# Kernel optimization log

Measured on AMD Instinct MI355X. Metric: run time of the kernel, lower is better.

## Reference

```python
import jax, jax.numpy as jnp
import numpy as np

HIDDEN = 512
LAYERS = 3
K = 8
EPS = 1e-5


def build_adjacency(coords, k):
    # squared pairwise distances (monotone in cdist, so same top-k indices)
    sq = jnp.sum(coords * coords, axis=-1)                      # [B,N]
    d2 = sq[:, :, None] + sq[:, None, :] - 2.0 * jnp.einsum('bnc,bmc->bnm', coords, coords)
    _, idx = jax.lax.top_k(-d2, k + 1)                          # smallest k+1
    idx = idx[:, :, 1:]                                         # drop self  [B,N,k]
    B, N = coords.shape[:2]
    bidx = jnp.arange(B)[:, None, None]
    ridx = jnp.arange(N)[None, :, None]
    adj = jnp.zeros((B, N, N), coords.dtype).at[bidx, ridx, idx].set(1.0)
    adj = adj + jnp.swapaxes(adj, -2, -1)                       # symmetrize
    return (adj > 0).astype(coords.dtype)


def layer_norm(x, g, b):
    mu = jnp.mean(x, axis=-1, keepdims=True)
    var = jnp.var(x, axis=-1, keepdims=True)  # biased, matches torch LayerNorm
    return (x - mu) * jax.lax.rsqrt(var + EPS) * g + b


def setup_inputs() -> dict:
    key = jax.random.key(0)
    k1, k2, k3, k4 = jax.random.split(key, 4)
    B, N, H, L = 4, 4096, HIDDEN, LAYERS
    node_features = jax.random.normal(k1, (B, N, H), dtype=jnp.float32)
    coordinates = jax.random.uniform(k2, (B, N, 2), dtype=jnp.float32)
    scale = 1.0 / np.sqrt(H)
    W = jax.random.uniform(k3, (L, H, H), dtype=jnp.float32, minval=-scale, maxval=scale)
    b = jax.random.uniform(k4, (L, H), dtype=jnp.float32, minval=-scale, maxval=scale)
    gamma = jnp.ones((L, H), dtype=jnp.float32)
    beta = jnp.zeros((L, H), dtype=jnp.float32)
    return {"node_features": node_features, "coordinates": coordinates,
            "W": W, "b": b, "gamma": gamma, "beta": beta}


def reference(node_features, coordinates, W, b, gamma, beta):
    adj = build_adjacency(coordinates, K)                       # [B,N,N]
    x = node_features
    for i in range(LAYERS):
        x_new = jnp.einsum('bnm,bmh->bnh', adj, x)              # dense aggregate
        x_new = x_new @ W[i] + b[i]                             # linear
        x_new = jax.nn.relu(layer_norm(x_new, gamma[i], beta[i]))
        x = x + x_new if i > 0 else x_new
    return x
```

## Files before the change

kernel.cpp:

```cpp
#include <hip/hip_runtime.h>
#include <stdint.h>

#define HIDDEN 512
#define NLAYERS 3
#define KNN 8
#define CAP 64
#define EPSV 1e-5f
#define GRID 32
#define NCELL (GRID * GRID)

typedef unsigned long long u64;
typedef __attribute__((ext_vector_type(8))) short short8;
typedef __attribute__((ext_vector_type(4))) float f32x4;

__device__ inline unsigned short f2bf(float x) {
  union { float f; unsigned u; } v; v.f = x;
  unsigned r = v.u + 0x7FFFu + ((v.u >> 16) & 1u);
  return (unsigned short)(r >> 16);
}
__device__ inline float bf2f(unsigned short u) {
  return __uint_as_float((unsigned)u << 16);
}

__global__ __launch_bounds__(1024) void grid_build_kernel(
    const float2* __restrict__ coords, int* __restrict__ cell_start,
    float2* __restrict__ scoord, int* __restrict__ sorig, int N) {
  __shared__ int hist[NCELL];
  __shared__ int offs[NCELL];
  int b = blockIdx.x;
  int t = threadIdx.x;
  hist[t] = 0;
  __syncthreads();
  const float2* cb = coords + (size_t)b * N;
  int mycell[4];
#pragma unroll
  for (int r = 0; r < 4; ++r) {
    int i = t + r * 1024;
    float2 c = cb[i];
    int cx = (int)(c.x * GRID); cx = cx < 0 ? 0 : (cx > GRID - 1 ? GRID - 1 : cx);
    int cy = (int)(c.y * GRID); cy = cy < 0 ? 0 : (cy > GRID - 1 ? GRID - 1 : cy);
    mycell[r] = cy * GRID + cx;
    atomicAdd(&hist[mycell[r]], 1);
  }
  __syncthreads();
  int v = hist[t];
  offs[t] = v;
  __syncthreads();
  for (int d = 1; d < NCELL; d <<= 1) {
    int add = (t >= d) ? offs[t - d] : 0;
    __syncthreads();
    offs[t] += add;
    __syncthreads();
  }
  int excl = offs[t] - v;
  cell_start[(size_t)b * (NCELL + 1) + t] = excl;
  if (t == 0) cell_start[(size_t)b * (NCELL + 1) + NCELL] = N;
  hist[t] = excl;
  __syncthreads();
#pragma unroll
  for (int r = 0; r < 4; ++r) {
    int i = t + r * 1024;
    int pos = atomicAdd(&hist[mycell[r]], 1);
    scoord[(size_t)b * N + pos] = cb[i];
    sorig[(size_t)b * N + pos] = i;
  }
}

__global__ __launch_bounds__(256) void knn_grid_kernel(
    const int* __restrict__ cell_start, const float2* __restrict__ scoord,
    const int* __restrict__ sorig, int* __restrict__ knn_s, int N, int BN) {
  int gang = (blockIdx.x * blockDim.x + threadIdx.x) >> 3;
  int sub = threadIdx.x & 7;
  if (gang >= BN) return;
  int b = gang / N;
  float2 cn = scoord[gang];
  float sqn = __fmaf_rn(cn.y, cn.y, __fmul_rn(cn.x, cn.x));
  int cx = (int)(cn.x * GRID); cx = cx < 0 ? 0 : (cx > GRID - 1 ? GRID - 1 : cx);
  int cy = (int)(cn.y * GRID); cy = cy < 0 ? 0 : (cy > GRID - 1 ? GRID - 1 : cy);
  const int* cs = cell_start + (size_t)b * (NCELL + 1);
  const float2* sc = scoord + (size_t)b * N;
  const int* so = sorig + (size_t)b * N;

  u64 list[KNN + 1];
#pragma unroll
  for (int j = 0; j <= KNN; ++j) list[j] = ~0ull;

  auto scan_cell = [&](int ux, int uy) {
    int c = uy * GRID + ux;
    int s = cs[c], e = cs[c + 1];
    for (int p = s + sub; p < e; p += 8) {
      float2 cm = sc[p];
      float sqm = __fmaf_rn(cm.y, cm.y, __fmul_rn(cm.x, cm.x));
      float dot = __fmaf_rn(cn.y, cm.y, __fmul_rn(cn.x, cm.x));
      float d2 = __fsub_rn(__fadd_rn(sqn, sqm), __fmul_rn(2.0f, dot));
      unsigned ub = __float_as_uint(d2);
      unsigned k32 = (ub & 0x80000000u) ? ~ub : (ub | 0x80000000u);
      u64 key = ((u64)k32 << 24) | ((u64)(unsigned)so[p] << 12) | (u64)(unsigned)p;
      if (key < list[KNN]) {
        u64 cur = key;
#pragma unroll
        for (int j = 0; j <= KNN; ++j) {
          u64 lo = list[j] < cur ? list[j] : cur;
          u64 hi = list[j] < cur ? cur : list[j];
          list[j] = lo;
          cur = hi;
        }
      }
    }
  };

  for (int q = 0; q <= GRID; ++q) {
    if (q == 0) {
      scan_cell(cx, cy);
    } else {
      int x0 = cx - q, x1 = cx + q, y0 = cy - q, y1 = cy + q;
      int xa = x0 < 0 ? 0 : x0, xb_ = x1 > GRID - 1 ? GRID - 1 : x1;
      for (int ux = xa; ux <= xb_; ++ux) {
        if (y0 >= 0) scan_cell(ux, y0);
        if (y1 <= GRID - 1) scan_cell(ux, y1);
      }
      int ya = (y0 + 1) < 0 ? 0 : y0 + 1, yb = (y1 - 1) > GRID - 1 ? GRID - 1 : y1 - 1;
      for (int uy = ya; uy <= yb; ++uy) {
        if (x0 >= 0) scan_cell(x0, uy);
        if (x1 <= GRID - 1) scan_cell(x1, uy);
      }
      float bound = (float)q * (1.0f / GRID);
      float thr = bound * bound - 1e-5f;
      int cntn = 0;
#pragma unroll
      for (int j = 0; j <= KNN; ++j) {
        unsigned k32 = (unsigned)(list[j] >> 24);
        float d2v = (k32 >= 0x80000000u) ? __uint_as_float(k32 & 0x7FFFFFFFu)
                                         : -__uint_as_float(~k32);
        cntn += (list[j] != ~0ull && d2v < thr) ? 1 : 0;
      }
#pragma unroll
      for (int o = 1; o < 8; o <<= 1) cntn += __shfl_xor(cntn, o, 64);
      if (cntn >= 9) break;
    }
  }

  for (int r = 0; r <= KNN; ++r) {
    u64 cand = list[0];
    u64 mn = cand;
#pragma unroll
    for (int o = 1; o < 8; o <<= 1) {
      u64 v = __shfl_xor(mn, o, 64);
      mn = v < mn ? v : mn;
    }
    if (cand == mn) {
#pragma unroll
      for (int j = 0; j < KNN; ++j) list[j] = list[j + 1];
      list[KNN] = ~0ull;
      if (r > 0) knn_s[(size_t)gang * KNN + (r - 1)] = (int)(mn & 0xFFFull);
    }
  }
}

__global__ __launch_bounds__(256) void rev_build_kernel(const int* __restrict__ knn,
                                                        int* __restrict__ cnt,
                                                        int* __restrict__ rev,
                                                        int N, int BN) {
  int e = blockIdx.x * blockDim.x + threadIdx.x;
  if (e >= BN * KNN) return;
  int bn = e >> 3;
  int m = knn[e];
  int b = bn / N;
  int gm = b * N + m;
  int pos = atomicAdd(&cnt[gm], 1);
  if (pos < CAP) rev[(size_t)gm * CAP + pos] = bn - b * N;
}

__global__ __launch_bounds__(128) void x2bf_perm_kernel(const float* __restrict__ x,
                                                        const int* __restrict__ sorig,
                                                        unsigned short* __restrict__ xs,
                                                        int N) {
  int row = blockIdx.x;
  int b = row / N;
  int src = b * N + sorig[row];
  int t = threadIdx.x;
  float4 v = ((const float4*)(x + (size_t)src * HIDDEN))[t];
  ushort4 o;
  o.x = f2bf(v.x); o.y = f2bf(v.y); o.z = f2bf(v.z); o.w = f2bf(v.w);
  ((ushort4*)(xs + (size_t)row * HIDDEN))[t] = o;
}

__global__ __launch_bounds__(128) void agg_kernel(const unsigned short* __restrict__ x,
                                                  const int* __restrict__ knn,
                                                  const int* __restrict__ cnt,
                                                  const int* __restrict__ rev,
                                                  unsigned short* __restrict__ aggb,
                                                  int N) {
  int bn = blockIdx.x;
  int b = bn / N;
  int t = threadIdx.x;
  const int* my = knn + (size_t)bn * KNN;
  int nb[KNN];
#pragma unroll
  for (int j = 0; j < KNN; ++j) nb[j] = my[j];
  const unsigned short* xb = x + (size_t)b * N * HIDDEN;
  float4 acc = {0.f, 0.f, 0.f, 0.f};
#pragma unroll
  for (int j = 0; j < KNN; ++j) {
    ushort4 v = ((const ushort4*)(xb + (size_t)nb[j] * HIDDEN))[t];
    acc.x += bf2f(v.x); acc.y += bf2f(v.y); acc.z += bf2f(v.z); acc.w += bf2f(v.w);
  }
  int indeg = cnt[bn];
  if (indeg > CAP) indeg = CAP;
  const int* rv = rev + (size_t)bn * CAP;
  for (int i = 0; i < indeg; ++i) {
    int r = rv[i];
    bool dup = false;
#pragma unroll
    for (int j = 0; j < KNN; ++j) dup = dup || (r == nb[j]);
    if (!dup) {
      ushort4 v = ((const ushort4*)(xb + (size_t)r * HIDDEN))[t];
      acc.x += bf2f(v.x); acc.y += bf2f(v.y); acc.z += bf2f(v.z); acc.w += bf2f(v.w);
    }
  }
  ushort4 o;
  o.x = f2bf(acc.x); o.y = f2bf(acc.y); o.z = f2bf(acc.z); o.w = f2bf(acc.w);
  ((ushort4*)(aggb + (size_t)bn * HIDDEN))[t] = o;
}

__global__ __launch_bounds__(256) void wconv_kernel(const float* __restrict__ W,
                                                    unsigned short* __restrict__ Wt) {
  __shared__ unsigned short tile[64][65];
  int l = blockIdx.x >> 6;
  int t6 = blockIdx.x & 63;
  int k0 = (t6 >> 3) * 64, n0 = (t6 & 7) * 64;
  const float* Wl = W + (size_t)l * HIDDEN * HIDDEN;
  unsigned short* Wtl = Wt + (size_t)l * HIDDEN * HIDDEN;
  int t = threadIdx.x;
#pragma unroll
  for (int r = 0; r < 4; ++r) {
    int row = (t >> 4) + r * 16;
    int col = (t & 15) * 4;
    float4 v = *(const float4*)(Wl + (size_t)(k0 + row) * HIDDEN + n0 + col);
    tile[col + 0][row] = f2bf(v.x);
    tile[col + 1][row] = f2bf(v.y);
    tile[col + 2][row] = f2bf(v.z);
    tile[col + 3][row] = f2bf(v.w);
  }
  __syncthreads();
#pragma unroll
  for (int r = 0; r < 4; ++r) {
    int row = (t >> 4) + r * 16;
    int col = (t & 15) * 4;
    ushort4 o;
    o.x = tile[row][col + 0]; o.y = tile[row][col + 1];
    o.z = tile[row][col + 2]; o.w = tile[row][col + 3];
    *(ushort4*)(Wtl + (size_t)(n0 + row) * HIDDEN + k0 + col) = o;
  }
}

__global__ __launch_bounds__(256) void gemm_mfma_kernel(
    const unsigned short* __restrict__ A,
    const unsigned short* __restrict__ Wt,
    const float* __restrict__ bias,
    float* __restrict__ C) {
  __shared__ unsigned short As[128 * 40];
  __shared__ unsigned short Bs[128 * 40];
  int t = threadIdx.x;
  int n0 = blockIdx.x * 128;
  int m0 = blockIdx.y * 128;
  int w = t >> 6, lane = t & 63;
  int wr = w >> 1, wc = w & 1;
  int lm = lane & 15, q = lane >> 4;

  f32x4 acc[4][4];
#pragma unroll
  for (int i = 0; i < 4; ++i)
#pragma unroll
    for (int j = 0; j < 4; ++j) acc[i][j] = (f32x4){0.f, 0.f, 0.f, 0.f};

  int srow = t >> 2;
  int scol = (t & 3) * 8;

  for (int k0 = 0; k0 < HIDDEN; k0 += 32) {
    uint4 a0 = *(const uint4*)(A + (size_t)(m0 + srow) * HIDDEN + k0 + scol);
    uint4 a1 = *(const uint4*)(A + (size_t)(m0 + srow + 64) * HIDDEN + k0 + scol);
    uint4 b0 = *(const uint4*)(Wt + (size_t)(n0 + srow) * HIDDEN + k0 + scol);
    uint4 b1 = *(const uint4*)(Wt + (size_t)(n0 + srow + 64) * HIDDEN + k0 + scol);
    __syncthreads();
    *(uint4*)(As + srow * 40 + scol) = a0;
    *(uint4*)(As + (srow + 64) * 40 + scol) = a1;
    *(uint4*)(Bs + srow * 40 + scol) = b0;
    *(uint4*)(Bs + (srow + 64) * 40 + scol) = b1;
    __syncthreads();
    short8 af[4], bfr[4];
#pragma unroll
    for (int i = 0; i < 4; ++i)
      af[i] = *(const short8*)(As + (wr * 64 + i * 16 + lm) * 40 + q * 8);
#pragma unroll
    for (int j = 0; j < 4; ++j)
      bfr[j] = *(const short8*)(Bs + (wc * 64 + j * 16 + lm) * 40 + q * 8);
#pragma unroll
    for (int i = 0; i < 4; ++i)
#pragma unroll
      for (int j = 0; j < 4; ++j)
        acc[i][j] = __builtin_amdgcn_mfma_f32_16x16x32_bf16(af[i], bfr[j], acc[i][j], 0, 0, 0);
  }

#pragma unroll
  for (int i = 0; i < 4; ++i) {
    int row = m0 + wr * 64 + i * 16 + q * 4;
#pragma unroll
    for (int j = 0; j < 4; ++j) {
      int col = n0 + wc * 64 + j * 16 + lm;
      float bv = bias[col];
#pragma unroll
      for (int r = 0; r < 4; ++r)
        C[(size_t)(row + r) * HIDDEN + col] = acc[i][j][r] + bv;
    }
  }
}

__global__ __launch_bounds__(256) void ln_relu_res_kernel(
    const float* __restrict__ t, const float* __restrict__ g,
    const float* __restrict__ be, unsigned short* __restrict__ xs,
    float* __restrict__ out, const int* __restrict__ sorig,
    int N, int addres, int final_) {
  int row = (blockIdx.x << 2) + (threadIdx.x >> 6);
  int lane = threadIdx.x & 63;
  const float4* tr = (const float4*)(t + (size_t)row * HIDDEN);
  float4 v0 = tr[lane];
  float4 v1 = tr[lane + 64];
  float s = ((v0.x + v0.y) + (v0.z + v0.w)) + ((v1.x + v1.y) + (v1.z + v1.w));
  float ss = ((v0.x * v0.x + v0.y * v0.y) + (v0.z * v0.z + v0.w * v0.w)) +
             ((v1.x * v1.x + v1.y * v1.y) + (v1.z * v1.z + v1.w * v1.w));
#pragma unroll
  for (int o = 32; o > 0; o >>= 1) {
    s += __shfl_xor(s, o, 64);
    ss += __shfl_xor(ss, o, 64);
  }
  float mu = s * (1.0f / HIDDEN);
  float var = ss * (1.0f / HIDDEN) - mu * mu;
  float inv = rsqrtf(var + EPSV);
  float4 g0 = ((const float4*)g)[lane], g1 = ((const float4*)g)[lane + 64];
  float4 b0 = ((const float4*)be)[lane], b1 = ((const float4*)be)[lane + 64];
  float4 o0, o1;
  o0.x = fmaxf((v0.x - mu) * inv * g0.x + b0.x, 0.f);
  o0.y = fmaxf((v0.y - mu) * inv * g0.y + b0.y, 0.f);
  o0.z = fmaxf((v0.z - mu) * inv * g0.z + b0.z, 0.f);
  o0.w = fmaxf((v0.w - mu) * inv * g0.w + b0.w, 0.f);
  o1.x = fmaxf((v1.x - mu) * inv * g1.x + b1.x, 0.f);
  o1.y = fmaxf((v1.y - mu) * inv * g1.y + b1.y, 0.f);
  o1.z = fmaxf((v1.z - mu) * inv * g1.z + b1.z, 0.f);
  o1.w = fmaxf((v1.w - mu) * inv * g1.w + b1.w, 0.f);
  ushort4* xrow = (ushort4*)(xs + (size_t)row * HIDDEN);
  if (addres) {
    ushort4 r0 = xrow[lane], r1 = xrow[lane + 64];
    o0.x += bf2f(r0.x); o0.y += bf2f(r0.y); o0.z += bf2f(r0.z); o0.w += bf2f(r0.w);
    o1.x += bf2f(r1.x); o1.y += bf2f(r1.y); o1.z += bf2f(r1.z); o1.w += bf2f(r1.w);
  }
  if (final_) {
    int b = row / N;
    int dst = b * N + sorig[row];
    float4* orow = (float4*)(out + (size_t)dst * HIDDEN);
    orow[lane] = o0;
    orow[lane + 64] = o1;
  } else {
    ushort4 q0, q1;
    q0.x = f2bf(o0.x); q0.y = f2bf(o0.y); q0.z = f2bf(o0.z); q0.w = f2bf(o0.w);
    q1.x = f2bf(o1.x); q1.y = f2bf(o1.y); q1.z = f2bf(o1.z); q1.w = f2bf(o1.w);
    xrow[lane] = q0;
    xrow[lane + 64] = q1;
  }
}

extern "C" void kernel_launch(void* const* d_in, const int* in_sizes, int n_in,
                              void* d_out, int out_size, void* d_ws, size_t ws_size,
                              hipStream_t stream) {
  const float* nf = (const float*)d_in[0];
  const float2* coords = (const float2*)d_in[1];
  const float* Wall = (const float*)d_in[2];
  const float* ball = (const float*)d_in[3];
  const float* gall = (const float*)d_in[4];
  const float* beall = (const float*)d_in[5];
  float* out = (float*)d_out;

  int BN = in_sizes[0] / HIDDEN;
  int N = 4096;
  int B = BN / N;

  char* ws = (char*)d_ws;
  size_t off = 0;
  auto alloc = [&](size_t bytes) -> void* {
    off = (off + 255) & ~(size_t)255;
    void* p = ws + off;
    off += bytes;
    return p;
  };
  int* knn_s = (int*)alloc((size_t)BN * KNN * sizeof(int));
  int* cnt = (int*)alloc((size_t)BN * sizeof(int));
  int* rev = (int*)alloc((size_t)BN * CAP * sizeof(int));
  unsigned short* aggb = (unsigned short*)alloc((size_t)BN * HIDDEN * sizeof(unsigned short));
  float* tmp = (float*)alloc((size_t)BN * HIDDEN * sizeof(float));
  unsigned short* Wt = (unsigned short*)alloc((size_t)NLAYERS * HIDDEN * HIDDEN * sizeof(unsigned short));
  unsigned short* xs = (unsigned short*)alloc((size_t)BN * HIDDEN * sizeof(unsigned short));
  int* cell_start = (int*)alloc((size_t)B * (NCELL + 1) * sizeof(int));
  float2* scoord = (float2*)alloc((size_t)BN * sizeof(float2));
  int* sorig = (int*)alloc((size_t)BN * sizeof(int));

  hipMemsetAsync(cnt, 0, (size_t)BN * sizeof(int), stream);
  grid_build_kernel<<<B, 1024, 0, stream>>>(coords, cell_start, scoord, sorig, N);
  knn_grid_kernel<<<(BN * 8 + 255) / 256, 256, 0, stream>>>(cell_start, scoord, sorig, knn_s, N, BN);
  rev_build_kernel<<<(BN * KNN) / 256, 256, 0, stream>>>(knn_s, cnt, rev, N, BN);
  wconv_kernel<<<NLAYERS * 64, 256, 0, stream>>>(Wall, Wt);
  x2bf_perm_kernel<<<BN, 128, 0, stream>>>(nf, sorig, xs, N);

  for (int l = 0; l < NLAYERS; ++l) {
    agg_kernel<<<BN, 128, 0, stream>>>(xs, knn_s, cnt, rev, aggb, N);
    gemm_mfma_kernel<<<dim3(HIDDEN / 128, BN / 128), 256, 0, stream>>>(
        aggb, Wt + (size_t)l * HIDDEN * HIDDEN, ball + (size_t)l * HIDDEN, tmp);
    ln_relu_res_kernel<<<BN / 4, 256, 0, stream>>>(
        tmp, gall + (size_t)l * HIDDEN, beall + (size_t)l * HIDDEN,
        xs, out, sorig, N, l > 0, l == NLAYERS - 1);
  }
}
```

Measured before the change: 296.4 us.

## Fuse GEMM with LayerNorm, ReLU and residual using full-row tiles

Replaces the separate GEMM and LayerNorm/ReLU/residual kernels with one kernel where each 512-thread block computes 64 full output rows across all 512 columns. Row statistics are reduced with shuffles and shared memory, then normalization, ReLU, residual add and output stores happen from registers. This removes the fp32 intermediate buffer's write and read plus a launch. In exchange, each block reloads the entire weight slice, the grid shrinks to fewer, larger blocks, and epilogue stores are narrow and strided.

```diff
diff --git a/kernel.cpp b/kernel.cpp
--- a/kernel.cpp
+++ b/kernel.cpp
@@ -254,18 +254,22 @@
   }
 }
 
-__global__ __launch_bounds__(256) void gemm_mfma_kernel(
+__global__ __launch_bounds__(512) void gemm_ln_fused_kernel(
     const unsigned short* __restrict__ A,
     const unsigned short* __restrict__ Wt,
     const float* __restrict__ bias,
-    float* __restrict__ C) {
-  __shared__ unsigned short As[128 * 40];
-  __shared__ unsigned short Bs[128 * 40];
+    const float* __restrict__ g,
+    const float* __restrict__ be,
+    unsigned short* __restrict__ xs,
+    float* __restrict__ out,
+    const int* __restrict__ sorig,
+    int N, int addres, int final_) {
+  __shared__ unsigned short As[64 * 40];
+  __shared__ unsigned short Bs[512 * 40];
+  __shared__ float red[8][64][2];
   int t = threadIdx.x;
-  int n0 = blockIdx.x * 128;
-  int m0 = blockIdx.y * 128;
+  int m0 = blockIdx.x * 64;
   int w = t >> 6, lane = t & 63;
-  int wr = w >> 1, wc = w & 1;
   int lm = lane & 15, q = lane >> 4;
 
   f32x4 acc[4][4];
@@ -274,98 +278,114 @@
 #pragma unroll
     for (int j = 0; j < 4; ++j) acc[i][j] = (f32x4){0.f, 0.f, 0.f, 0.f};
 
-  int srow = t >> 2;
-  int scol = (t & 3) * 8;
+  int arow = t >> 2;
+  int acol = (t & 3) * 8;
+  int brow0 = t >> 2;
+  int bcol = (t & 3) * 8;
 
   for (int k0 = 0; k0 < HIDDEN; k0 += 32) {
-    uint4 a0 = *(const uint4*)(A + (size_t)(m0 + srow) * HIDDEN + k0 + scol);
-    uint4 a1 = *(const uint4*)(A + (size_t)(m0 + srow + 64) * HIDDEN + k0 + scol);
-    uint4 b0 = *(const uint4*)(Wt + (size_t)(n0 + srow) * HIDDEN + k0 + scol);
-    uint4 b1 = *(const uint4*)(Wt + (size_t)(n0 + srow + 64) * HIDDEN + k0 + scol);
+    uint4 av;
+    if (t < 256) av = *(const uint4*)(A + (size_t)(m0 + arow) * HIDDEN + k0 + acol);
+    uint4 bv[4];
+#pragma unroll
+    for (int r = 0; r < 4; ++r)
+      bv[r] = *(const uint4*)(Wt + (size_t)(brow0 + r * 128) * HIDDEN + k0 + bcol);
     __syncthreads();
-    *(uint4*)(As + srow * 40 + scol) = a0;
-    *(uint4*)(As + (srow + 64) * 40 + scol) = a1;
-    *(uint4*)(Bs + srow * 40 + scol) = b0;
-    *(uint4*)(Bs + (srow + 64) * 40 + scol) = b1;
+    if (t < 256) *(uint4*)(As + arow * 40 + acol) = av;
+#pragma unroll
+    for (int r = 0; r < 4; ++r)
+      *(uint4*)(Bs + (brow0 + r * 128) * 40 + bcol) = bv[r];
     __syncthreads();
-    short8 af[4], bfr[4];
+    short8 af[4], bf[4];
 #pragma unroll
     for (int i = 0; i < 4; ++i)
-      af[i] = *(const short8*)(As + (wr * 64 + i * 16 + lm) * 40 + q * 8);
+      af[i] = *(const short8*)(As + (i * 16 + lm) * 40 + q * 8);
 #pragma unroll
     for (int j = 0; j < 4; ++j)
-      bfr[j] = *(const short8*)(Bs + (wc * 64 + j * 16 + lm) * 40 + q * 8);
+      bf[j] = *(const short8*)(Bs + (w * 64 + j * 16 + lm) * 40 + q * 8);
 #pragma unroll
     for (int i = 0; i < 4; ++i)
 #pragma unroll
       for (int j = 0; j < 4; ++j)
-        acc[i][j] = __builtin_amdgcn_mfma_f32_16x16x32_bf16(af[i], bfr[j], acc[i][j], 0, 0, 0);
-  }
+        acc[i][j] = __builtin_amdgcn_mfma_f32_16x16x32_bf16(af[i], bf[j], acc[i][j], 0, 0, 0);
+  }
+
+  float bv4[4], gv[4], bev[4];
+#pragma unroll
+  for (int j = 0; j < 4; ++j) {
+    int col = w * 64 + j * 16 + lm;
+    bv4[j] = bias[col]; gv[j] = g[col]; bev[j] = be[col];
+  }
+  float s[4][4], ss[4][4];
+#pragma unroll
+  for (int i = 0; i < 4; ++i)
+#pragma unroll
+    for (int r = 0; r < 4; ++r) { s[i][r] = 0.f; ss[i][r] = 0.f; }
+#pragma unroll
+  for (int i = 0; i < 4; ++i)
+#pragma unroll
+    for (int j = 0; j < 4; ++j)
+#pragma unroll
+      for (int r = 0; r < 4; ++r) {
+        float v = acc[i][j][r] + bv4[j];
+        acc[i][j][r] = v;
+        s[i][r] += v;
+        ss[i][r] += v * v;
+      }
+#pragma unroll
+  for (int i = 0; i < 4; ++i)
+#pragma unroll
+    for (int r = 0; r < 4; ++r) {
+#pragma unroll
+      for (int o = 1; o < 16; o <<= 1) {
+        s[i][r] += __shfl_xor(s[i][r], o, 64);
+        ss[i][r] += __shfl_xor(ss[i][r], o, 64);
+      }
+    }
+  if (lm == 0) {
+#pragma unroll
+    for (int i = 0; i < 4; ++i)
+#pragma unroll
+      for (int r = 0; r < 4; ++r) {
+        int rloc = i * 16 + q * 4 + r;
+        red[w][rloc][0] = s[i][r];
+        red[w][rloc][1] = ss[i][r];
+      }
+  }
+  __syncthreads();
 
 #pragma unroll
   for (int i = 0; i < 4; ++i) {
-    int row = m0 + wr * 64 + i * 16 + q * 4;
-#pragma unroll
-    for (int j = 0; j < 4; ++j) {
-      int col = n0 + wc * 64 + j * 16 + lm;
-      float bv = bias[col];
-#pragma unroll
-      for (int r = 0; r < 4; ++r)
-        C[(size_t)(row + r) * HIDDEN + col] = acc[i][j][r] + bv;
-    }
-  }
-}
-
-__global__ __launch_bounds__(256) void ln_relu_res_kernel(
-    const float* __restrict__ t, const float* __restrict__ g,
-    const float* __restrict__ be, unsigned short* __restrict__ xs,
-    float* __restrict__ out, const int* __restrict__ sorig,
-    int N, int addres, int final_) {
-  int row = (blockIdx.x << 2) + (threadIdx.x >> 6);
-  int lane = threadIdx.x & 63;
-  const float4* tr = (const float4*)(t + (size_t)row * HIDDEN);
-  float4 v0 = tr[lane];
-  float4 v1 = tr[lane + 64];
-  float s = ((v0.x + v0.y) + (v0.z + v0.w)) + ((v1.x + v1.y) + (v1.z + v1.w));
-  float ss = ((v0.x * v0.x + v0.y * v0.y) + (v0.z * v0.z + v0.w * v0.w)) +
-             ((v1.x * v1.x + v1.y * v1.y) + (v1.z * v1.z + v1.w * v1.w));
-#pragma unroll
-  for (int o = 32; o > 0; o >>= 1) {
-    s += __shfl_xor(s, o, 64);
-    ss += __shfl_xor(ss, o, 64);
-  }
-  float mu = s * (1.0f / HIDDEN);
-  float var = ss * (1.0f / HIDDEN) - mu * mu;
-  float inv = rsqrtf(var + EPSV);
-  float4 g0 = ((const float4*)g)[lane], g1 = ((const float4*)g)[lane + 64];
-  float4 b0 = ((const float4*)be)[lane], b1 = ((const float4*)be)[lane + 64];
-  float4 o0, o1;
-  o0.x = fmaxf((v0.x - mu) * inv * g0.x + b0.x, 0.f);
-  o0.y = fmaxf((v0.y - mu) * inv * g0.y + b0.y, 0.f);
-  o0.z = fmaxf((v0.z - mu) * inv * g0.z + b0.z, 0.f);
-  o0.w = fmaxf((v0.w - mu) * inv * g0.w + b0.w, 0.f);
-  o1.x = fmaxf((v1.x - mu) * inv * g1.x + b1.x, 0.f);
-  o1.y = fmaxf((v1.y - mu) * inv * g1.y + b1.y, 0.f);
-  o1.z = fmaxf((v1.z - mu) * inv * g1.z + b1.z, 0.f);
-  o1.w = fmaxf((v1.w - mu) * inv * g1.w + b1.w, 0.f);
-  ushort4* xrow = (ushort4*)(xs + (size_t)row * HIDDEN);
-  if (addres) {
-    ushort4 r0 = xrow[lane], r1 = xrow[lane + 64];
-    o0.x += bf2f(r0.x); o0.y += bf2f(r0.y); o0.z += bf2f(r0.z); o0.w += bf2f(r0.w);
-    o1.x += bf2f(r1.x); o1.y += bf2f(r1.y); o1.z += bf2f(r1.z); o1.w += bf2f(r1.w);
-  }
-  if (final_) {
-    int b = row / N;
-    int dst = b * N + sorig[row];
-    float4* orow = (float4*)(out + (size_t)dst * HIDDEN);
-    orow[lane] = o0;
-    orow[lane + 64] = o1;
-  } else {
-    ushort4 q0, q1;
-    q0.x = f2bf(o0.x); q0.y = f2bf(o0.y); q0.z = f2bf(o0.z); q0.w = f2bf(o0.w);
-    q1.x = f2bf(o1.x); q1.y = f2bf(o1.y); q1.z = f2bf(o1.z); q1.w = f2bf(o1.w);
-    xrow[lane] = q0;
-    xrow[lane + 64] = q1;
+#pragma unroll
+    for (int r = 0; r < 4; ++r) {
+      int rloc = i * 16 + q * 4 + r;
+      float S = 0.f, SS = 0.f;
+#pragma unroll
+      for (int ww = 0; ww < 8; ++ww) { S += red[ww][rloc][0]; SS += red[ww][rloc][1]; }
+      float mu = S * (1.0f / HIDDEN);
+      float var = SS * (1.0f / HIDDEN) - mu * mu;
+      float inv = rsqrtf(var + EPSV);
+      int row_g = m0 + rloc;
+      if (final_) {
+        int bb = row_g / N;
+        size_t dst = (size_t)(bb * N + sorig[row_g]) * HIDDEN;
+#pragma unroll
+        for (int j = 0; j < 4; ++j) {
+          int col = w * 64 + j * 16 + lm;
+          float v = fmaxf((acc[i][j][r] - mu) * inv * gv[j] + bev[j], 0.f);
+          if (addres) v += bf2f(xs[(size_t)row_g * HIDDEN + col]);
+          out[dst + col] = v;
+        }
+      } else {
+#pragma unroll
+        for (int j = 0; j < 4; ++j) {
+          int col = w * 64 + j * 16 + lm;
+          float v = fmaxf((acc[i][j][r] - mu) * inv * gv[j] + bev[j], 0.f);
+          if (addres) v += bf2f(xs[(size_t)row_g * HIDDEN + col]);
+          xs[(size_t)row_g * HIDDEN + col] = f2bf(v);
+        }
+      }
+    }
   }
 }
 
@@ -396,7 +416,6 @@
   int* cnt = (int*)alloc((size_t)BN * sizeof(int));
   int* rev = (int*)alloc((size_t)BN * CAP * sizeof(int));
   unsigned short* aggb = (unsigned short*)alloc((size_t)BN * HIDDEN * sizeof(unsigned short));
-  float* tmp = (float*)alloc((size_t)BN * HIDDEN * sizeof(float));
   unsigned short* Wt = (unsigned short*)alloc((size_t)NLAYERS * HIDDEN * HIDDEN * sizeof(unsigned short));
   unsigned short* xs = (unsigned short*)alloc((size_t)BN * HIDDEN * sizeof(unsigned short));
   int* cell_start = (int*)alloc((size_t)B * (NCELL + 1) * sizeof(int));
@@ -412,10 +431,9 @@
 
   for (int l = 0; l < NLAYERS; ++l) {
     agg_kernel<<<BN, 128, 0, stream>>>(xs, knn_s, cnt, rev, aggb, N);
-    gemm_mfma_kernel<<<dim3(HIDDEN / 128, BN / 128), 256, 0, stream>>>(
-        aggb, Wt + (size_t)l * HIDDEN * HIDDEN, ball + (size_t)l * HIDDEN, tmp);
-    ln_relu_res_kernel<<<BN / 4, 256, 0, stream>>>(
-        tmp, gall + (size_t)l * HIDDEN, beall + (size_t)l * HIDDEN,
+    gemm_ln_fused_kernel<<<BN / 64, 512, 0, stream>>>(
+        aggb, Wt + (size_t)l * HIDDEN * HIDDEN, ball + (size_t)l * HIDDEN,
+        gall + (size_t)l * HIDDEN, beall + (size_t)l * HIDDEN,
         xs, out, sorig, N, l > 0, l == NLAYERS - 1);
   }
 }
```

After: 391.5 us. 1.32x slower.
